# Kernel tuning notes

Measured on AMD Instinct MI355X. Metric: run time of the kernel, lower is better.

## Reference

```python
import jax, jax.numpy as jnp
import numpy as np

N = 262144      # total atoms (ragged over batch)
B = 64          # batch_size
K = 16          # retrieved features per sample
H = 256         # h_dim
R = 512         # ret_feat_dim


def setup_inputs() -> dict:
    key = jax.random.key(0)
    k1, k2, k3, k4, k5, k6, k7 = jax.random.split(key, 7)
    h = jax.random.normal(k1, (N, H), dtype=jnp.float32)
    ret_feat = jax.random.normal(k2, (B, K, R), dtype=jnp.float32)
    batch = jnp.sort(jax.random.randint(k3, (N,), 0, B, dtype=jnp.int64))
    # nn.Linear weights: y = x @ W.T + b
    Wp = jax.random.normal(k4, (H, R), dtype=jnp.float32) / np.sqrt(R)
    bp = jax.random.normal(k5, (H,), dtype=jnp.float32) * 0.01
    Wl = jax.random.normal(k6, (H, 2 * H), dtype=jnp.float32) / np.sqrt(2 * H)
    bl = jax.random.normal(k7, (H,), dtype=jnp.float32) * 0.01
    return {"h": h, "ret_feat": ret_feat, "batch": batch,
            "Wp": Wp, "bp": bp, "Wl": Wl, "bl": bl}


def reference(h, ret_feat, batch, Wp, bp, Wl, bl):
    # ret_feat: [B, K, R] -> mean over K -> project to [B, H]
    ret = jnp.mean(ret_feat, axis=1)                    # [B, R]
    ret = ret @ Wp.T + bp                               # [B, H]
    # The torch loop gathers h[batch==i], concats the pooled feature
    # repeated per atom, applies `linear`, and scatters back. Since every
    # atom is covered exactly once, this is a per-node gather + linear:
    per_node = ret[batch]                               # [N, H] gather
    x = jnp.concatenate([h, per_node], axis=-1)         # [N, 2H]
    return x @ Wl.T + bl                                # [N, H]
```

## Files before the change

### kernel.cpp

```cpp
#include <hip/hip_runtime.h>
#include <hip/hip_bf16.h>

#define N_ATOMS 262144
#define B_SZ    64
#define H_DIM   256
#define R_DIM   512

#define TILE_ROWS 32
#define TPB       16
#define NBLOCKS   (N_ATOMS / (TILE_ROWS * TPB))

typedef __attribute__((ext_vector_type(8))) short bf16x8;
typedef __attribute__((ext_vector_type(4))) float f32x4;

static __device__ __forceinline__ short f2bf(float f) {
  unsigned u = __builtin_bit_cast(unsigned, f);
  u = (u + 0x7FFFu + ((u >> 16) & 1u)) >> 16;
  return (short)u;
}

static __device__ __forceinline__ unsigned cvtpk(float lo, float hi) {
  unsigned r;
  asm("v_cvt_pk_bf16_f32 %0, %1, %2" : "=v"(r) : "v"(lo), "v"(hi));
  return r;
}

static __device__ __forceinline__ bf16x8 pack8(f32x4 a0, f32x4 a1) {
  unsigned u0 = cvtpk(a0[0], a0[1]);
  unsigned u1 = cvtpk(a0[2], a0[3]);
  unsigned u2 = cvtpk(a1[0], a1[1]);
  unsigned u3 = cvtpk(a1[2], a1[3]);
  bf16x8 v;
  v[0] = (short)(u0 & 0xFFFF); v[1] = (short)(u0 >> 16);
  v[2] = (short)(u1 & 0xFFFF); v[3] = (short)(u1 >> 16);
  v[4] = (short)(u2 & 0xFFFF); v[5] = (short)(u2 >> 16);
  v[6] = (short)(u3 & 0xFFFF); v[7] = (short)(u3 >> 16);
  return v;
}

static __device__ __forceinline__ void async_copy16(const float* g, short* lds) {
  __builtin_amdgcn_global_load_lds(
      (const __attribute__((address_space(1))) unsigned int*)g,
      (__attribute__((address_space(3))) unsigned int*)lds,
      16, 0, 0);
}

__global__ __launch_bounds__(1024) void prep_kernel(
    const float* __restrict__ rf, const float* __restrict__ Wp,
    const float* __restrict__ bp, const float* __restrict__ Wl,
    const float* __restrict__ bl, float* __restrict__ pooled,
    short* __restrict__ Bbf) {
  int t = threadIdx.x;
  if (blockIdx.x >= B_SZ) {
    int base = (blockIdx.x - B_SZ) * 4096 + t * 4;
#pragma unroll
    for (int q = 0; q < 4; ++q) {
      int idx  = base + q;
      int j    = idx & 7;
      int lane = (idx >> 3) & 63;
      int ks   = (idx >> 9) & 7;
      int ct   = idx >> 12;
      int o    = ct * 16 + (lane & 15);
      int k    = ks * 32 + ((lane >> 4) << 3) + j;
      Bbf[idx] = f2bf(Wl[o * (2 * H_DIM) + k]);
    }
    return;
  }

  __shared__ float meanr[R_DIM];
  __shared__ float retj[H_DIM];
  int b    = blockIdx.x;
  int lane = t & 63;
  int w    = t >> 6;

  if (t < R_DIM) {
    float s = 0.f;
    const float* p = rf + (long)b * 16 * R_DIM + t;
#pragma unroll
    for (int k = 0; k < 16; ++k) s += p[k * R_DIM];
    meanr[t] = s * (1.f / 16.f);
  }
  __syncthreads();

  {
    f32x4 m0 = *(const f32x4*)&meanr[lane * 8];
    f32x4 m1 = *(const f32x4*)&meanr[lane * 8 + 4];
#pragma unroll
    for (int jj = 0; jj < 16; ++jj) {
      int j = w * 16 + jj;
      const f32x4* wp = (const f32x4*)(Wp + (long)j * R_DIM + lane * 8);
      f32x4 w0 = wp[0], w1 = wp[1];
      float s = m0[0]*w0[0] + m0[1]*w0[1] + m0[2]*w0[2] + m0[3]*w0[3]
              + m1[0]*w1[0] + m1[1]*w1[1] + m1[2]*w1[2] + m1[3]*w1[3];
#pragma unroll
      for (int d = 1; d < 64; d <<= 1) s += __shfl_xor(s, d);
      if (lane == 0) retj[j] = s + bp[j];
    }
  }
  __syncthreads();

  {
    f32x4 r0 = *(const f32x4*)&retj[lane * 4];
#pragma unroll
    for (int oo = 0; oo < 16; ++oo) {
      int o = w * 16 + oo;
      f32x4 wv = *(const f32x4*)(Wl + (long)o * (2 * H_DIM) + H_DIM + lane * 4);
      float s = r0[0]*wv[0] + r0[1]*wv[1] + r0[2]*wv[2] + r0[3]*wv[3];
#pragma unroll
      for (int d = 1; d < 64; d <<= 1) s += __shfl_xor(s, d);
      if (lane == 0) pooled[b * H_DIM + o] = s + bl[o];
    }
  }
}

__global__ __launch_bounds__(512, 4) void gemm_kernel(
    const float* __restrict__ h, const short* __restrict__ Bbf,
    const float* __restrict__ pooled, const int* __restrict__ batch,
    float* __restrict__ out) {
  __shared__ short As[2][32 * 512];
  int t    = threadIdx.x;
  int lane = t & 63;
  int w    = t >> 6;
  const int arow = lane & 15;
  const int kg   = lane >> 4;

  bf16x8 bfrag0[8], bfrag1[8];
#pragma unroll
  for (int ks = 0; ks < 8; ++ks) {
    bfrag0[ks] = *(const bf16x8*)(Bbf + ((((2 * w)     * 8 + ks) * 64 + lane) << 3));
    bfrag1[ks] = *(const bf16x8*)(Bbf + ((((2 * w + 1) * 8 + ks) * 64 + lane) << 3));
  }

  int S_[4], row_[4], col_[4];
#pragma unroll
  for (int i = 0; i < 4; ++i) {
    int S   = 4 * w + i;
    S_[i]   = S;
    row_[i] = ((S >> 4) << 4) + arow;
    col_[i] = (((S >> 1) & 7) << 5) + (kg << 3) + ((S & 1) << 2);
  }

  long base_row = (long)blockIdx.x * (TILE_ROWS * TPB);

#pragma unroll
  for (int i = 0; i < 4; ++i)
    async_copy16(h + (base_row + row_[i]) * H_DIM + col_[i],
                 &As[0][S_[i] * 512]);
  __syncthreads();

  int o0 = ((2 * w) << 4) + (kg << 2);
  int o1 = o0 + 16;

  for (int tt = 0; tt < TPB; ++tt) {
    int  buf = tt & 1;
    long g0  = base_row + (long)tt * TILE_ROWS;

    if (tt + 1 < TPB) {
      long gn = g0 + TILE_ROWS;
#pragma unroll
      for (int i = 0; i < 4; ++i)
        async_copy16(h + (gn + row_[i]) * H_DIM + col_[i],
                     &As[buf ^ 1][S_[i] * 512]);
    }

#pragma unroll
    for (int rt = 0; rt < 2; ++rt) {
      f32x4 acc0 = {0.f, 0.f, 0.f, 0.f};
      f32x4 acc1 = {0.f, 0.f, 0.f, 0.f};
#pragma unroll
      for (int ks = 0; ks < 8; ++ks) {
        int S0 = rt * 16 + ks * 2;
        f32x4 v0 = *(const f32x4*)&As[buf][(S0 * 512) + lane * 8];
        f32x4 v1 = *(const f32x4*)&As[buf][((S0 + 1) * 512) + lane * 8];
        bf16x8 af = pack8(v0, v1);
        acc0 = __builtin_amdgcn_mfma_f32_16x16x32_bf16(bfrag0[ks], af, acc0, 0, 0, 0);
        acc1 = __builtin_amdgcn_mfma_f32_16x16x32_bf16(bfrag1[ks], af, acc1, 0, 0, 0);
      }
      long row = g0 + rt * 16 + arow;
      int  b   = batch[row];
      const float* pb = pooled + b * H_DIM;
      f32x4 pv0 = *(const f32x4*)(pb + o0);
      f32x4 pv1 = *(const f32x4*)(pb + o1);
      float* orow = out + row * H_DIM;
      *(f32x4*)(orow + o0) = acc0 + pv0;
      *(f32x4*)(orow + o1) = acc1 + pv1;
    }

    __syncthreads();
  }
}

extern "C" void kernel_launch(void* const* d_in, const int* in_sizes, int n_in,
                              void* d_out, int out_size, void* d_ws, size_t ws_size,
                              hipStream_t stream) {
  const float* h   = (const float*)d_in[0];
  const float* rf  = (const float*)d_in[1];
  const int*   bat = (const int*)d_in[2];
  const float* Wp  = (const float*)d_in[3];
  const float* bp  = (const float*)d_in[4];
  const float* Wl  = (const float*)d_in[5];
  const float* bl  = (const float*)d_in[6];
  float* out = (float*)d_out;

  float* pooled = (float*)d_ws;
  short* Bbf    = (short*)((char*)d_ws + 64 * 1024);

  prep_kernel<<<B_SZ + 16, 1024, 0, stream>>>(rf, Wp, bp, Wl, bl, pooled, Bbf);
  gemm_kernel<<<NBLOCKS, 512, 0, stream>>>(h, Bbf, pooled, bat, out);
}
```

Before: 149.3 us.

## Deepen GEMM pipeline to 4-stage async LDS ring with prefetched batch/pooled loads

The GEMM kernel now works on 16-row tiles through a 4-buffer LDS ring, prefetching h three tiles ahead. It uses explicit vmcnt waits and raw barriers instead of __syncthreads. The batch index and pooled-row loads are software-pipelined one or two tiles ahead, so the gather latency stays off the critical path. This trades more hand-tuned wait-count bookkeeping, which is fragile if the compiler reorders memory ops, for fewer exposed global-load stalls per tile.

```diff
diff --git a/kernel.cpp b/kernel.cpp
--- a/kernel.cpp
+++ b/kernel.cpp
@@ -6,9 +6,10 @@
 #define H_DIM   256
 #define R_DIM   512
 
-#define TILE_ROWS 32
-#define TPB       16
+#define TILE_ROWS 16
+#define TPB       32
 #define NBLOCKS   (N_ATOMS / (TILE_ROWS * TPB))
+#define NBUF      4
 
 typedef __attribute__((ext_vector_type(8))) short bf16x8;
 typedef __attribute__((ext_vector_type(4))) float f32x4;
@@ -117,7 +118,7 @@
     const float* __restrict__ h, const short* __restrict__ Bbf,
     const float* __restrict__ pooled, const int* __restrict__ batch,
     float* __restrict__ out) {
-  __shared__ short As[2][32 * 512];
+  __shared__ short As[NBUF][16 * 512];
   int t    = threadIdx.x;
   int lane = t & 63;
   int w    = t >> 6;
@@ -131,62 +132,76 @@
     bfrag1[ks] = *(const bf16x8*)(Bbf + ((((2 * w + 1) * 8 + ks) * 64 + lane) << 3));
   }
 
-  int S_[4], row_[4], col_[4];
-#pragma unroll
-  for (int i = 0; i < 4; ++i) {
-    int S   = 4 * w + i;
-    S_[i]   = S;
-    row_[i] = ((S >> 4) << 4) + arow;
-    col_[i] = (((S >> 1) & 7) << 5) + (kg << 3) + ((S & 1) << 2);
-  }
-
   long base_row = (long)blockIdx.x * (TILE_ROWS * TPB);
-
-#pragma unroll
-  for (int i = 0; i < 4; ++i)
-    async_copy16(h + (base_row + row_[i]) * H_DIM + col_[i],
-                 &As[0][S_[i] * 512]);
-  __syncthreads();
-
-  int o0 = ((2 * w) << 4) + (kg << 2);
+  int o0 = (w << 5) + (kg << 2);
   int o1 = o0 + 16;
+  const long lsrc = (long)arow * H_DIM + (w << 5) + (kg << 3);
+
+  int b_cur = batch[base_row + arow];
+  {
+    const float* gp = h + base_row * H_DIM + lsrc;
+    async_copy16(gp,     &As[0][(2 * w) * 512]);
+    async_copy16(gp + 4, &As[0][(2 * w + 1) * 512]);
+  }
+  f32x4 pv0, pv1;
+  {
+    const float* pb = pooled + b_cur * H_DIM;
+    pv0 = *(const f32x4*)(pb + o0);
+    pv1 = *(const f32x4*)(pb + o1);
+  }
+  int b_next = batch[base_row + TILE_ROWS + arow];
+#pragma unroll
+  for (int tl = 1; tl <= 2; ++tl) {
+    const float* gp = h + (base_row + (long)tl * TILE_ROWS) * H_DIM + lsrc;
+    async_copy16(gp,     &As[tl][(2 * w) * 512]);
+    async_copy16(gp + 4, &As[tl][(2 * w + 1) * 512]);
+  }
+  asm volatile("s_waitcnt vmcnt(4)" ::: "memory");
+  __builtin_amdgcn_s_barrier();
+  __builtin_amdgcn_sched_barrier(0);
 
   for (int tt = 0; tt < TPB; ++tt) {
-    int  buf = tt & 1;
-    long g0  = base_row + (long)tt * TILE_ROWS;
-
+    long g0 = base_row + (long)tt * TILE_ROWS;
+
+    f32x4 npv0 = {0.f, 0.f, 0.f, 0.f}, npv1 = {0.f, 0.f, 0.f, 0.f};
     if (tt + 1 < TPB) {
-      long gn = g0 + TILE_ROWS;
-#pragma unroll
-      for (int i = 0; i < 4; ++i)
-        async_copy16(h + (gn + row_[i]) * H_DIM + col_[i],
-                     &As[buf ^ 1][S_[i] * 512]);
-    }
-
-#pragma unroll
-    for (int rt = 0; rt < 2; ++rt) {
-      f32x4 acc0 = {0.f, 0.f, 0.f, 0.f};
-      f32x4 acc1 = {0.f, 0.f, 0.f, 0.f};
-#pragma unroll
-      for (int ks = 0; ks < 8; ++ks) {
-        int S0 = rt * 16 + ks * 2;
-        f32x4 v0 = *(const f32x4*)&As[buf][(S0 * 512) + lane * 8];
-        f32x4 v1 = *(const f32x4*)&As[buf][((S0 + 1) * 512) + lane * 8];
-        bf16x8 af = pack8(v0, v1);
-        acc0 = __builtin_amdgcn_mfma_f32_16x16x32_bf16(bfrag0[ks], af, acc0, 0, 0, 0);
-        acc1 = __builtin_amdgcn_mfma_f32_16x16x32_bf16(bfrag1[ks], af, acc1, 0, 0, 0);
-      }
-      long row = g0 + rt * 16 + arow;
-      int  b   = batch[row];
-      const float* pb = pooled + b * H_DIM;
-      f32x4 pv0 = *(const f32x4*)(pb + o0);
-      f32x4 pv1 = *(const f32x4*)(pb + o1);
-      float* orow = out + row * H_DIM;
-      *(f32x4*)(orow + o0) = acc0 + pv0;
-      *(f32x4*)(orow + o1) = acc1 + pv1;
-    }
-
-    __syncthreads();
+      const float* pb = pooled + b_next * H_DIM;
+      npv0 = *(const f32x4*)(pb + o0);
+      npv1 = *(const f32x4*)(pb + o1);
+    }
+    int b_next2 = 0;
+    if (tt + 2 < TPB) b_next2 = batch[g0 + 2 * TILE_ROWS + arow];
+    if (tt + 3 < TPB) {
+      const float* gp = h + (g0 + 3 * TILE_ROWS) * H_DIM + lsrc;
+      short* dst = &As[(tt + 3) & 3][0];
+      async_copy16(gp,     dst + (2 * w) * 512);
+      async_copy16(gp + 4, dst + (2 * w + 1) * 512);
+    }
+    __builtin_amdgcn_sched_barrier(0);
+    asm volatile("s_waitcnt vmcnt(9)" ::: "memory");
+    __builtin_amdgcn_sched_barrier(0);
+
+    const short* ab = &As[tt & 3][0];
+    f32x4 acc0 = {0.f, 0.f, 0.f, 0.f};
+    f32x4 acc1 = {0.f, 0.f, 0.f, 0.f};
+#pragma unroll
+    for (int ks = 0; ks < 8; ++ks) {
+      f32x4 v0 = *(const f32x4*)(ab + ks * 1024 + lane * 8);
+      f32x4 v1 = *(const f32x4*)(ab + ks * 1024 + 512 + lane * 8);
+      bf16x8 af = pack8(v0, v1);
+      acc0 = __builtin_amdgcn_mfma_f32_16x16x32_bf16(bfrag0[ks], af, acc0, 0, 0, 0);
+      acc1 = __builtin_amdgcn_mfma_f32_16x16x32_bf16(bfrag1[ks], af, acc1, 0, 0, 0);
+    }
+    float* orow = out + (g0 + arow) * H_DIM;
+    *(f32x4*)(orow + o0) = acc0 + pv0;
+    *(f32x4*)(orow + o1) = acc1 + pv1;
+
+    pv0 = npv0; pv1 = npv1; b_next = b_next2;
+
+    if (tt + 1 < TPB) {
+      __builtin_amdgcn_s_barrier();
+      __builtin_amdgcn_sched_barrier(0);
+    }
   }
 }
 
```

New measurement: 146.1 us. 2.1% less time.
